# Performance work log

Hardware: AMD Instinct MI355X
Metric: run time of the kernel (lower is better)

The kernel has to match this reference:

```python
import jax, jax.numpy as jnp
import numpy as np
from jax import lax

H = 51  # hidden size hardcoded in SequenceLSTM


def setup_inputs() -> dict:
    key = jax.random.key(0)
    ks = jax.random.split(key, 12)
    B, T = 256, 2048
    init = lambda k, sh: jax.random.normal(k, sh, dtype=jnp.float32) * 0.08
    return {
        "x": jax.random.normal(ks[0], (B, T), dtype=jnp.float32),
        "W_ih1": init(ks[1], (4 * H, 1)),
        "W_hh1": init(ks[2], (4 * H, H)),
        "b_ih1": init(ks[3], (4 * H,)),
        "b_hh1": init(ks[4], (4 * H,)),
        "W_ih2": init(ks[5], (4 * H, H)),
        "W_hh2": init(ks[6], (4 * H, H)),
        "b_ih2": init(ks[7], (4 * H,)),
        "b_hh2": init(ks[8], (4 * H,)),
        "fc_w": init(ks[9], (1, H)),
        "fc_b": init(ks[10], (1,)),
        "future": 64,
    }


def _cell(xt, h, c, Wih, Whh, bih, bhh):
    # PyTorch LSTMCell: gates in order i, f, g, o
    g = xt @ Wih.T + h @ Whh.T + (bih + bhh)
    i, f, gg, o = jnp.split(g, 4, axis=-1)
    c = jax.nn.sigmoid(f) * c + jax.nn.sigmoid(i) * jnp.tanh(gg)
    h = jax.nn.sigmoid(o) * jnp.tanh(c)
    return h, c


def reference(x, W_ih1, W_hh1, b_ih1, b_hh1, W_ih2, W_hh2, b_ih2, b_hh2,
              fc_w, fc_b, future):
    B = x.shape[0]
    z = jnp.zeros((B, H), dtype=x.dtype)

    def step(carry, xt):  # xt: [B, 1]
        h1, c1, h2, c2 = carry
        h1, c1 = _cell(xt, h1, c1, W_ih1, W_hh1, b_ih1, b_hh1)
        h2, c2 = _cell(h1, h2, c2, W_ih2, W_hh2, b_ih2, b_hh2)
        out = h2 @ fc_w.T + fc_b  # [B, 1]
        return (h1, c1, h2, c2), out

    carry, outs = lax.scan(step, (z, z, z, z), x.T[:, :, None])  # outs: [T, B, 1]

    if future > 0:
        def fstep(carry, _):
            h1, c1, h2, c2, out = carry
            h1, c1 = _cell(out, h1, c1, W_ih1, W_hh1, b_ih1, b_hh1)
            h2, c2 = _cell(h1, h2, c2, W_ih2, W_hh2, b_ih2, b_hh2)
            out = h2 @ fc_w.T + fc_b
            return (h1, c1, h2, c2, out), out

        fcarry = (*carry, outs[-1])
        _, fouts = lax.scan(fstep, fcarry, None, length=future)
        outs = jnp.concatenate([outs, fouts], axis=0)

    return outs[:, :, 0].T  # [B, T + future]
```

## Files before the change

kernel.cpp:

```cpp
#include <hip/hip_runtime.h>

#define H 51

__device__ __forceinline__ float rl_(float v, int lane) {
    return __builtin_bit_cast(float, __builtin_amdgcn_readlane(__builtin_bit_cast(int, v), lane));
}
template<int CTRL>
__device__ __forceinline__ float qb_(float v) {
    return __builtin_bit_cast(float, __builtin_amdgcn_update_dpp(
        0, __builtin_bit_cast(int, v), CTRL, 0xf, 0xf, true));
}

__device__ __forceinline__ float act_(float x, float m2, float A, float B) {
    const float e = __builtin_amdgcn_exp2f(m2 * x);
    const float r = __builtin_amdgcn_rcpf(1.f + e);
    return fmaf(A, r, B);
}
__device__ __forceinline__ float tanh_(float c) {
    const float e = __builtin_amdgcn_exp2f(2.885390082f * c);
    const float r = __builtin_amdgcn_rcpf(1.f + e);
    return fmaf(-2.f, r, 1.f);
}

__global__ __launch_bounds__(256, 1)
void lstm_seq_kernel(const float* __restrict__ x,
                     const float* __restrict__ Wih1, const float* __restrict__ Whh1,
                     const float* __restrict__ bih1, const float* __restrict__ bhh1,
                     const float* __restrict__ Wih2, const float* __restrict__ Whh2,
                     const float* __restrict__ bih2, const float* __restrict__ bhh2,
                     const float* __restrict__ fcw, const float* __restrict__ fcb,
                     float* __restrict__ out, int T, int future)
{
    const int b   = blockIdx.x;
    const int tid = threadIdx.x;
    const int l   = tid & 63;
    const int w   = tid >> 6;
    const int uq  = l >> 2;
    const int g   = l & 3;
    const int u   = 13 * w + uq;
    const bool act_lane = (uq < 13) && (u < H);
    const bool g0lane   = act_lane && (g == 0);

    extern __shared__ float xld[];
    __shared__ float h1s[2][64];
    __shared__ float h2s[2][64];
    __shared__ __align__(16) float fcp[4];

    for (int i = tid; i < T; i += 256) xld[i] = x[(size_t)b * T + i];
    if (tid < 64) { h1s[0][tid] = 0.f; h1s[1][tid] = 0.f;
                    h2s[0][tid] = 0.f; h2s[1][tid] = 0.f; }
    if (tid < 4) fcp[tid] = 0.f;

    const int row = g * H + u;
    const float wx1   = act_lane ? Wih1[row] : 0.f;
    const float bias1 = act_lane ? (bih1[row] + bhh1[row]) : 0.f;
    const float bias2 = act_lane ? (bih2[row] + bhh2[row]) : 0.f;
    const float fcu   = g0lane ? fcw[u] : 0.f;
    const float fcb_l = fcb[0];

    const float m2A = (g == 2) ? 2.885390082f : -1.442695041f;
    const float Aa  = act_lane ? ((g == 2) ? -2.f : 1.f) : 0.f;
    const float Ba  = (act_lane && g == 2) ? 1.f : 0.f;

    float w1[H], w2i[H], w2h[H];
    #pragma unroll
    for (int k = 0; k < H; ++k) {
        w1[k]  = act_lane ? Whh1[(size_t)row * H + k] : 0.f;
        w2i[k] = act_lane ? Wih2[(size_t)row * H + k] : 0.f;
        w2h[k] = act_lane ? Whh2[(size_t)row * H + k] : 0.f;
    }
    #pragma unroll
    for (int k = 0; k < H; ++k)
        asm volatile("" : "+v"(w1[k]), "+v"(w2i[k]), "+v"(w2h[k]));

    float c1 = 0.f, c2 = 0.f;
    __syncthreads();

    const int TT = T + future;
    for (int t = 0; t < TT; ++t) {
        const int p = t & 1, q = p ^ 1;

        float xt;
        {
            float o = 0.f;
            if (t > 0) {
                const float4 f = *(const float4*)fcp;
                o = (f.x + f.y) + (f.z + f.w) + fcb_l;
                if (tid == 0) out[(size_t)b * TT + (t - 1)] = o;
            }
            xt = (t < T) ? xld[t] : o;
        }

        const float h1v = h1s[q][l];
        const float h2v = h2s[q][l];

        float a0 = 0.f, a1 = 0.f, a2 = 0.f, a3 = 0.f;
        float d0 = 0.f, d1 = 0.f, d2 = 0.f, d3 = 0.f;
        #pragma unroll
        for (int k = 0; k < 48; k += 4) {
            a0 = fmaf(rl_(h1v, k + 0), w1[k + 0], a0);
            a1 = fmaf(rl_(h1v, k + 1), w1[k + 1], a1);
            a2 = fmaf(rl_(h1v, k + 2), w1[k + 2], a2);
            a3 = fmaf(rl_(h1v, k + 3), w1[k + 3], a3);
            d0 = fmaf(rl_(h2v, k + 0), w2h[k + 0], d0);
            d1 = fmaf(rl_(h2v, k + 1), w2h[k + 1], d1);
            d2 = fmaf(rl_(h2v, k + 2), w2h[k + 2], d2);
            d3 = fmaf(rl_(h2v, k + 3), w2h[k + 3], d3);
        }
        a0 = fmaf(rl_(h1v, 48), w1[48], a0);
        a1 = fmaf(rl_(h1v, 49), w1[49], a1);
        a2 = fmaf(rl_(h1v, 50), w1[50], a2);
        d0 = fmaf(rl_(h2v, 48), w2h[48], d0);
        d1 = fmaf(rl_(h2v, 49), w2h[49], d1);
        d2 = fmaf(rl_(h2v, 50), w2h[50], d2);

        const float pre1 = bias1 + fmaf(wx1, xt, (a0 + a1) + (a2 + a3));
        const float hh2  = (d0 + d1) + (d2 + d3);

        float act = act_(pre1, m2A, Aa, Ba);
        {
            const float si = qb_<0x00>(act);
            const float sf = qb_<0x55>(act);
            const float tg = qb_<0xAA>(act);
            const float so = qb_<0xFF>(act);
            c1 = fmaf(sf, c1, si * tg);
            const float h1n = so * tanh_(c1);
            if (g0lane) h1s[p][u] = h1n;
        }
        __syncthreads();

        const float h1vp = h1s[p][l];
        float e0 = 0.f, e1 = 0.f, e2 = 0.f, e3 = 0.f;
        #pragma unroll
        for (int k = 0; k < 48; k += 4) {
            e0 = fmaf(rl_(h1vp, k + 0), w2i[k + 0], e0);
            e1 = fmaf(rl_(h1vp, k + 1), w2i[k + 1], e1);
            e2 = fmaf(rl_(h1vp, k + 2), w2i[k + 2], e2);
            e3 = fmaf(rl_(h1vp, k + 3), w2i[k + 3], e3);
        }
        e0 = fmaf(rl_(h1vp, 48), w2i[48], e0);
        e1 = fmaf(rl_(h1vp, 49), w2i[49], e1);
        e2 = fmaf(rl_(h1vp, 50), w2i[50], e2);

        const float pre2 = bias2 + hh2 + ((e0 + e1) + (e2 + e3));
        act = act_(pre2, m2A, Aa, Ba);
        {
            const float si = qb_<0x00>(act);
            const float sf = qb_<0x55>(act);
            const float tg = qb_<0xAA>(act);
            const float so = qb_<0xFF>(act);
            c2 = fmaf(sf, c2, si * tg);
            const float h2n = so * tanh_(c2);
            if (g0lane) h2s[p][u] = h2n;

            float pv = g0lane ? h2n * fcu : 0.f;
            pv += __shfl_xor(pv, 4, 64);
            pv += __shfl_xor(pv, 8, 64);
            pv += __shfl_xor(pv, 16, 64);
            pv += __shfl_xor(pv, 32, 64);
            if (l == 0) fcp[w] = pv;
        }
        __syncthreads();
    }

    if (tid == 0) {
        const float4 f = *(const float4*)fcp;
        out[(size_t)b * TT + (TT - 1)] = (f.x + f.y) + (f.z + f.w) + fcb_l;
    }
}

extern "C" void kernel_launch(void* const* d_in, const int* in_sizes, int n_in,
                              void* d_out, int out_size, void* d_ws, size_t ws_size,
                              hipStream_t stream) {
    const float* x    = (const float*)d_in[0];
    const float* Wih1 = (const float*)d_in[1];
    const float* Whh1 = (const float*)d_in[2];
    const float* bih1 = (const float*)d_in[3];
    const float* bhh1 = (const float*)d_in[4];
    const float* Wih2 = (const float*)d_in[5];
    const float* Whh2 = (const float*)d_in[6];
    const float* bih2 = (const float*)d_in[7];
    const float* bhh2 = (const float*)d_in[8];
    const float* fcw  = (const float*)d_in[9];
    const float* fcb  = (const float*)d_in[10];
    float* out = (float*)d_out;

    const int B  = 256;
    const int T  = in_sizes[0] / B;
    const int TT = out_size / B;
    const int future = TT - T;

    const size_t shmem = (size_t)T * sizeof(float);
    hipLaunchKernelGGL(lstm_seq_kernel, dim3(B), dim3(256), shmem, stream,
                       x, Wih1, Whh1, bih1, bhh1, Wih2, Whh2, bih2, bhh2,
                       fcw, fcb, out, T, future);
}
```

Measured before the change: 2.642 ms.

## Split LSTM weight matrices across three wave groups per block

Launches 768 threads per block and gives each group of four waves one weight matrix (Whh1, Whh2, Wih2) instead of having every wave hold all three. Layer-1 cell update and the h2 recurrent dot product run concurrently in phase one, with the recurrent part handed to phase two through a shared buffer. This cuts per-thread register weights from 153 to 51 and shortens the serial critical path per step. The cost is more waves per block and idle waves in each phase.

New measurement: 2.367 ms. 1.12x faster.

```diff
diff --git a/kernel.cpp b/kernel.cpp
--- a/kernel.cpp
+++ b/kernel.cpp
@@ -22,7 +22,22 @@
     return fmaf(-2.f, r, 1.f);
 }
 
-__global__ __launch_bounds__(256, 1)
+__device__ __forceinline__ float dot51_(const float* wt, float hv) {
+    float a0 = 0.f, a1 = 0.f, a2 = 0.f, a3 = 0.f;
+    #pragma unroll
+    for (int k = 0; k < 48; k += 4) {
+        a0 = fmaf(rl_(hv, k + 0), wt[k + 0], a0);
+        a1 = fmaf(rl_(hv, k + 1), wt[k + 1], a1);
+        a2 = fmaf(rl_(hv, k + 2), wt[k + 2], a2);
+        a3 = fmaf(rl_(hv, k + 3), wt[k + 3], a3);
+    }
+    a0 = fmaf(rl_(hv, 48), wt[48], a0);
+    a1 = fmaf(rl_(hv, 49), wt[49], a1);
+    a2 = fmaf(rl_(hv, 50), wt[50], a2);
+    return (a0 + a1) + (a2 + a3);
+}
+
+__global__ __launch_bounds__(768, 1)
 void lstm_seq_kernel(const float* __restrict__ x,
                      const float* __restrict__ Wih1, const float* __restrict__ Whh1,
                      const float* __restrict__ bih1, const float* __restrict__ bhh1,
@@ -35,122 +50,87 @@
     const int tid = threadIdx.x;
     const int l   = tid & 63;
     const int w   = tid >> 6;
+    const int grp = w >> 2;
+    const int j   = w & 3;
     const int uq  = l >> 2;
     const int g   = l & 3;
-    const int u   = 13 * w + uq;
+    const int u   = 13 * j + uq;
     const bool act_lane = (uq < 13) && (u < H);
     const bool g0lane   = act_lane && (g == 0);
+    const int row = act_lane ? (g * H + u) : 0;
 
     extern __shared__ float xld[];
     __shared__ float h1s[2][64];
     __shared__ float h2s[2][64];
+    __shared__ float hh2buf[208];
     __shared__ __align__(16) float fcp[4];
 
-    for (int i = tid; i < T; i += 256) xld[i] = x[(size_t)b * T + i];
+    for (int i = tid; i < T; i += 768) xld[i] = x[(size_t)b * T + i];
     if (tid < 64) { h1s[0][tid] = 0.f; h1s[1][tid] = 0.f;
                     h2s[0][tid] = 0.f; h2s[1][tid] = 0.f; }
     if (tid < 4) fcp[tid] = 0.f;
 
-    const int row = g * H + u;
-    const float wx1   = act_lane ? Wih1[row] : 0.f;
-    const float bias1 = act_lane ? (bih1[row] + bhh1[row]) : 0.f;
-    const float bias2 = act_lane ? (bih2[row] + bhh2[row]) : 0.f;
-    const float fcu   = g0lane ? fcw[u] : 0.f;
+    const float* Wm = (grp == 0) ? Whh1 : ((grp == 1) ? Whh2 : Wih2);
+    float wt[H];
+    #pragma unroll
+    for (int k = 0; k < H; ++k)
+        wt[k] = act_lane ? Wm[(size_t)row * H + k] : 0.f;
+
+    const float wx1   = (grp == 0 && act_lane) ? Wih1[row] : 0.f;
+    const float bias1 = (grp == 0 && act_lane) ? (bih1[row] + bhh1[row]) : 0.f;
+    const float bias2 = (grp == 2 && act_lane) ? (bih2[row] + bhh2[row]) : 0.f;
+    const float fcu   = (grp == 2 && g0lane) ? fcw[u] : 0.f;
     const float fcb_l = fcb[0];
 
     const float m2A = (g == 2) ? 2.885390082f : -1.442695041f;
     const float Aa  = act_lane ? ((g == 2) ? -2.f : 1.f) : 0.f;
     const float Ba  = (act_lane && g == 2) ? 1.f : 0.f;
 
-    float w1[H], w2i[H], w2h[H];
-    #pragma unroll
-    for (int k = 0; k < H; ++k) {
-        w1[k]  = act_lane ? Whh1[(size_t)row * H + k] : 0.f;
-        w2i[k] = act_lane ? Wih2[(size_t)row * H + k] : 0.f;
-        w2h[k] = act_lane ? Whh2[(size_t)row * H + k] : 0.f;
-    }
-    #pragma unroll
-    for (int k = 0; k < H; ++k)
-        asm volatile("" : "+v"(w1[k]), "+v"(w2i[k]), "+v"(w2h[k]));
-
-    float c1 = 0.f, c2 = 0.f;
+    float cc = 0.f;
     __syncthreads();
 
     const int TT = T + future;
     for (int t = 0; t < TT; ++t) {
         const int p = t & 1, q = p ^ 1;
 
-        float xt;
-        {
-            float o = 0.f;
-            if (t > 0) {
-                const float4 f = *(const float4*)fcp;
-                o = (f.x + f.y) + (f.z + f.w) + fcb_l;
-                if (tid == 0) out[(size_t)b * TT + (t - 1)] = o;
-            }
-            xt = (t < T) ? xld[t] : o;
+        float o = 0.f;
+        if (t > 0) {
+            const float4 f = *(const float4*)fcp;
+            o = (f.x + f.y) + (f.z + f.w) + fcb_l;
+            if (tid == 0) out[(size_t)b * TT + (t - 1)] = o;
         }
 
-        const float h1v = h1s[q][l];
-        const float h2v = h2s[q][l];
-
-        float a0 = 0.f, a1 = 0.f, a2 = 0.f, a3 = 0.f;
-        float d0 = 0.f, d1 = 0.f, d2 = 0.f, d3 = 0.f;
-        #pragma unroll
-        for (int k = 0; k < 48; k += 4) {
-            a0 = fmaf(rl_(h1v, k + 0), w1[k + 0], a0);
-            a1 = fmaf(rl_(h1v, k + 1), w1[k + 1], a1);
-            a2 = fmaf(rl_(h1v, k + 2), w1[k + 2], a2);
-            a3 = fmaf(rl_(h1v, k + 3), w1[k + 3], a3);
-            d0 = fmaf(rl_(h2v, k + 0), w2h[k + 0], d0);
-            d1 = fmaf(rl_(h2v, k + 1), w2h[k + 1], d1);
-            d2 = fmaf(rl_(h2v, k + 2), w2h[k + 2], d2);
-            d3 = fmaf(rl_(h2v, k + 3), w2h[k + 3], d3);
-        }
-        a0 = fmaf(rl_(h1v, 48), w1[48], a0);
-        a1 = fmaf(rl_(h1v, 49), w1[49], a1);
-        a2 = fmaf(rl_(h1v, 50), w1[50], a2);
-        d0 = fmaf(rl_(h2v, 48), w2h[48], d0);
-        d1 = fmaf(rl_(h2v, 49), w2h[49], d1);
-        d2 = fmaf(rl_(h2v, 50), w2h[50], d2);
-
-        const float pre1 = bias1 + fmaf(wx1, xt, (a0 + a1) + (a2 + a3));
-        const float hh2  = (d0 + d1) + (d2 + d3);
-
-        float act = act_(pre1, m2A, Aa, Ba);
-        {
-            const float si = qb_<0x00>(act);
-            const float sf = qb_<0x55>(act);
-            const float tg = qb_<0xAA>(act);
-            const float so = qb_<0xFF>(act);
-            c1 = fmaf(sf, c1, si * tg);
-            const float h1n = so * tanh_(c1);
+        if (grp == 0) {
+            const float xt = (t < T) ? xld[t] : o;
+            const float hv = h1s[q][l];
+            const float pre1 = bias1 + fmaf(wx1, xt, dot51_(wt, hv));
+            const float a = act_(pre1, m2A, Aa, Ba);
+            const float si = qb_<0x00>(a);
+            const float sf = qb_<0x55>(a);
+            const float tg = qb_<0xAA>(a);
+            const float so = qb_<0xFF>(a);
+            cc = fmaf(sf, cc, si * tg);
+            const float h1n = so * tanh_(cc);
             if (g0lane) h1s[p][u] = h1n;
+        } else if (grp == 1) {
+            const float hv = h2s[q][l];
+            const float hh2 = dot51_(wt, hv);
+            if (act_lane) hh2buf[52 * j + l] = hh2;
         }
         __syncthreads();
 
-        const float h1vp = h1s[p][l];
-        float e0 = 0.f, e1 = 0.f, e2 = 0.f, e3 = 0.f;
-        #pragma unroll
-        for (int k = 0; k < 48; k += 4) {
-            e0 = fmaf(rl_(h1vp, k + 0), w2i[k + 0], e0);
-            e1 = fmaf(rl_(h1vp, k + 1), w2i[k + 1], e1);
-            e2 = fmaf(rl_(h1vp, k + 2), w2i[k + 2], e2);
-            e3 = fmaf(rl_(h1vp, k + 3), w2i[k + 3], e3);
-        }
-        e0 = fmaf(rl_(h1vp, 48), w2i[48], e0);
-        e1 = fmaf(rl_(h1vp, 49), w2i[49], e1);
-        e2 = fmaf(rl_(h1vp, 50), w2i[50], e2);
-
-        const float pre2 = bias2 + hh2 + ((e0 + e1) + (e2 + e3));
-        act = act_(pre2, m2A, Aa, Ba);
-        {
-            const float si = qb_<0x00>(act);
-            const float sf = qb_<0x55>(act);
-            const float tg = qb_<0xAA>(act);
-            const float so = qb_<0xFF>(act);
-            c2 = fmaf(sf, c2, si * tg);
-            const float h2n = so * tanh_(c2);
+        if (grp == 2) {
+            const float hv = h1s[p][l];
+            const float dot = dot51_(wt, hv);
+            const float hh2 = act_lane ? hh2buf[52 * j + l] : 0.f;
+            const float pre2 = bias2 + hh2 + dot;
+            const float a = act_(pre2, m2A, Aa, Ba);
+            const float si = qb_<0x00>(a);
+            const float sf = qb_<0x55>(a);
+            const float tg = qb_<0xAA>(a);
+            const float so = qb_<0xFF>(a);
+            cc = fmaf(sf, cc, si * tg);
+            const float h2n = so * tanh_(cc);
             if (g0lane) h2s[p][u] = h2n;
 
             float pv = g0lane ? h2n * fcu : 0.f;
@@ -158,7 +138,7 @@
             pv += __shfl_xor(pv, 8, 64);
             pv += __shfl_xor(pv, 16, 64);
             pv += __shfl_xor(pv, 32, 64);
-            if (l == 0) fcp[w] = pv;
+            if (l == 0) fcp[j] = pv;
         }
         __syncthreads();
     }
@@ -191,7 +171,7 @@
     const int future = TT - T;
 
     const size_t shmem = (size_t)T * sizeof(float);
-    hipLaunchKernelGGL(lstm_seq_kernel, dim3(B), dim3(256), shmem, stream,
+    hipLaunchKernelGGL(lstm_seq_kernel, dim3(B), dim3(768), shmem, stream,
                        x, Wih1, Whh1, bih1, bhh1, Wih2, Whh2, bih2, bhh2,
                        fcw, fcb, out, T, future);
 }
```
